# Optimization experiments

Measured on AMD Instinct MI355X. Metric: run time of the kernel, lower is better.

## Reference

```python
import jax, jax.numpy as jnp
import numpy as np
import math

MAXL = 2; C = 16; A = 32; B = 2; LAYERS = 2; CUT = 0.5


def _cg_coeff(l1, l2, l, m1, m2, m):
    if m1 + m2 != m or l < abs(l1 - l2) or l > l1 + l2:
        return 0.0
    f = math.factorial
    pre = math.sqrt((2 * l + 1) * f(l + l1 - l2) * f(l - l1 + l2) * f(l1 + l2 - l) / f(l1 + l2 + l + 1))
    pre *= math.sqrt(f(l + m) * f(l - m) * f(l1 + m1) * f(l1 - m1) * f(l2 + m2) * f(l2 - m2))
    s = 0.0
    for k in range(0, l1 + l2 + 1):
        d = (k, l1 + l2 - l - k, l1 - m1 - k, l2 + m2 - k, l - l2 + m1 + k, l - l1 - m2 + k)
        if min(d) < 0:
            continue
        s += (-1.0) ** k / (f(d[0]) * f(d[1]) * f(d[2]) * f(d[3]) * f(d[4]) * f(d[5]))
    return pre * s


def _cg_matrix(l1, l2, l):
    M = np.zeros((2 * l1 + 1, 2 * l2 + 1, 2 * l + 1), dtype=np.float32)
    for m1 in range(-l1, l1 + 1):
        for m2 in range(-l2, l2 + 1):
            m = m1 + m2
            if -l <= m <= l:
                M[m1 + l1, m2 + l2, m + l] = _cg_coeff(l1, l2, l, m1, m2, m)
    return M

_CG = {}
for _l1 in range(MAXL + 1):
    for _l2 in range(MAXL + 1):
        for _l in range(abs(_l1 - _l2), min(_l1 + _l2, MAXL) + 1):
            _CG[(_l1, _l2, _l)] = jnp.asarray(_cg_matrix(_l1, _l2, _l))


def _cg_product(parts1, parts2):
    # GElib-style CG product: channel dim is the outer product of input channels,
    # concatenated over valid (l1,l2) couplings in loop order.
    out = [[] for _ in range(MAXL + 1)]
    for l1, p1 in enumerate(parts1):
        for l2, p2 in enumerate(parts2):
            for l in range(abs(l1 - l2), min(l1 + l2, MAXL) + 1):
                t = jnp.einsum('xyz,...xc,...yd->...zcd', _CG[(l1, l2, l)], p1, p2)
                out[l].append(t.reshape(t.shape[:-2] + (t.shape[-2] * t.shape[-1],)))
    return [jnp.concatenate(o, axis=-1) for o in out]


def _sph(rel_pos):
    # Real spherical harmonics (orthonormal convention) of the normalized rel vector,
    # broadcast across the C channels of type_sph.
    eps = 1e-6
    r = jnp.sqrt(jnp.sum(rel_pos * rel_pos, axis=-1, keepdims=True) + eps)
    u = rel_pos / r
    x, y, z = u[..., 0], u[..., 1], u[..., 2]
    Y0 = 0.28209479 * jnp.ones_like(x)[..., None]
    Y1 = 0.48860251 * jnp.stack([y, z, x], axis=-1)
    Y2 = jnp.stack([1.09254843 * x * y, 1.09254843 * y * z,
                    0.31539157 * (3.0 * z * z - 1.0), 1.09254843 * x * z,
                    0.54627422 * (x * x - y * y)], axis=-1)
    return [jnp.repeat(Y[..., None], C, axis=-1) for Y in (Y0, Y1, Y2)]


def _cg_layer(parts, conn, sph, wnl, wrel):
    # message pass: masked neighbor sum (Rmask1 gather)
    mp = [jnp.einsum('bij,bjomc->biomc', conn, p) for p in parts]
    cg_nl = _cg_product(mp, mp)
    mixed_nl = [jnp.einsum('baomt,aotc->baomc', p, w) for p, w in zip(cg_nl, wnl)]
    rep = [jnp.tile(p, (1, 1, A, 1, 1)) for p in mixed_nl]  # adims [A,1] -> [A,A]
    cg_rel = _cg_product(rep, sph)
    mixed_rel = [jnp.einsum('bijmt,ijtc->bijmc', p, w) for p, w in zip(cg_rel, wrel)]
    return [jnp.sum(p, axis=2, keepdims=True) for p in mixed_rel]


def _scalars(parts):
    b, a = parts[0].shape[0], parts[0].shape[1]
    s0 = parts[0].reshape(b, a, C)
    sn = [jnp.einsum('baomc,baomd->bacd', p, p).reshape(b, a, C * C) for p in parts]
    return jnp.concatenate([s0] + sn, axis=-1)


def setup_inputs() -> dict:
    key = jax.random.key(0)
    ks = jax.random.split(key, 20)
    tau_nl = [3 * C * C, 6 * C * C, 6 * C * C]
    inp = {
        'v0': jax.random.normal(ks[0], (B, A, 1, 1, C), jnp.float32),
        'v1': jax.random.normal(ks[1], (B, A, 1, 3, C), jnp.float32),
        'v2': jax.random.normal(ks[2], (B, A, 1, 5, C), jnp.float32),
        'rel_pos': jax.random.normal(ks[3], (B, A, A, 3), jnp.float32),
        'norms': jax.random.uniform(ks[4], (B, A, A), jnp.float32),
    }
    i = 5
    for layer in range(LAYERS):
        for l in range(MAXL + 1):
            inp['wnl%d_%d' % (layer, l)] = 0.02 * jax.random.normal(ks[i], (A, 1, tau_nl[l], C), jnp.float32); i += 1
            inp['wrel%d_%d' % (layer, l)] = 0.02 * jax.random.normal(ks[i], (A, A, tau_nl[l], C), jnp.float32); i += 1
    return inp


def reference(v0, v1, v2, rel_pos, norms,
              wnl0_0, wrel0_0, wnl0_1, wrel0_1, wnl0_2, wrel0_2,
              wnl1_0, wrel1_0, wnl1_1, wrel1_1, wnl1_2, wrel1_2):
    parts = [v0, v1, v2]
    sph = _sph(rel_pos)
    conn = (norms < CUT).astype(v0.dtype)
    wnl = [[wnl0_0, wnl0_1, wnl0_2], [wnl1_0, wnl1_1, wnl1_2]]
    wrel = [[wrel0_0, wrel0_1, wrel0_2], [wrel1_0, wrel1_1, wrel1_2]]
    outs = []
    for L in range(LAYERS):
        parts = _cg_layer(parts, conn, sph, wnl[L], wrel[L])
        outs.append(_scalars(parts))
    return jnp.concatenate(outs, axis=0)
```

## Files before the change

kernel.cpp:

```cpp
#include <hip/hip_runtime.h>

#define NA 32
#define NB 2
#define NC 16

constexpr int KL1[15]   = {0,1,2, 0,1,1,1,2,2, 0,1,1,2,2,2};
constexpr int KL2[15]   = {0,1,2, 1,0,1,2,1,2, 2,1,2,0,1,2};
constexpr int KOFF[15]  = {0,1,10, 35,44,53,80,125,170, 245,270,315,390,415,490};
constexpr int KLBASE[3] = {0,3,9};
constexpr int KLOFF[3]  = {0,1,4};
constexpr int KOFF3[3]  = {0,1024,4096};
__constant__ int CP_L1[15]   = {0,1,2, 0,1,1,1,2,2, 0,1,1,2,2,2};
__constant__ int CP_L2[15]   = {0,1,2, 1,0,1,2,1,2, 2,1,2,0,1,2};
__constant__ int CP_OFF[15]  = {0,1,10, 35,44,53,80,125,170, 245,270,315,390,415,490};
__constant__ int LBASE[3] = {0,3,9};
__constant__ int LOFF[3]  = {0,1,4};
__constant__ int OFF3[3]  = {0,1024,4096};

constexpr double cfact(int n){ double r=1.0; for(int i=2;i<=n;++i) r*=(double)i; return r; }
constexpr double csqrt(double x){
    double g = (x > 1.0) ? x : 1.0, prev = 0.0;
    for (int i = 0; i < 60 && g != prev; ++i) { prev = g; g = 0.5*(g + x/g); }
    return g;
}
struct CGT { float v[616]; };
constexpr CGT build_cg() {
    CGT t{};
    for (int cp=0; cp<15; ++cp){
        int l1=KL1[cp], l2=KL2[cp];
        int l = (cp<3)?0:((cp<9)?1:2);
        int n1=2*l1+1, n2=2*l2+1, nl=2*l+1;
        for (int x=0;x<n1;++x) for(int y=0;y<n2;++y) for(int z=0;z<nl;++z){
            int m1=x-l1, m2=y-l2, m=z-l;
            double val=0.0;
            if (m1+m2==m){
                double pre = csqrt((2.0*l+1.0)*cfact(l+l1-l2)*cfact(l-l1+l2)*cfact(l1+l2-l)/cfact(l1+l2+l+1));
                pre *= csqrt(cfact(l+m)*cfact(l-m)*cfact(l1+m1)*cfact(l1-m1)*cfact(l2+m2)*cfact(l2-m2));
                double s=0.0;
                for(int k=0;k<=l1+l2;++k){
                    int d0=k,d1=l1+l2-l-k,d2=l1-m1-k,d3=l2+m2-k,d4=l-l2+m1+k,d5=l-l1-m2+k;
                    if(d0<0||d1<0||d2<0||d3<0||d4<0||d5<0) continue;
                    double term = 1.0/(cfact(d0)*cfact(d1)*cfact(d2)*cfact(d3)*cfact(d4)*cfact(d5));
                    s += (k & 1) ? -term : term;
                }
                val = pre*s;
            }
            t.v[KOFF[cp] + (x*n2+y)*nl + z] = (float)val;
        }
    }
    return t;
}
__constant__ CGT CGC = build_cg();

template<int L>
__device__ void nl_body(int i, int b, int z,
    const float* __restrict__ p0, const float* __restrict__ p1, const float* __restrict__ p2,
    const float* __restrict__ norms, const float* __restrict__ wnl,
    float* __restrict__ mnl, float* smem)
{
    constexpr int MD  = 2*L+1;
    constexpr int TAU = (L == 0) ? 768 : 1536;
    constexpr int NK  = TAU / 256;

    float* shCG = smem;
    float* mp   = smem + 616;
    float* shcg = mp + 144;
    float* red  = shcg + TAU;

    const int tid = threadIdx.x;
    const int wave = tid >> 6, lane = tid & 63;

    for (int e = tid; e < 616; e += 256) shCG[e] = CGC.v[e];

    if (tid < 144) {
        int xt = tid >> 4, c = tid & 15;
        int lp = (xt < 1) ? 0 : ((xt < 4) ? 1 : 2);
        int x = xt - KLOFF[lp];
        int md = 2*lp+1;
        const float* pp = (lp == 0) ? p0 : ((lp == 1) ? p1 : p2);
        const float* nr = norms + (b*NA + i)*NA;
        float s = 0.0f;
#pragma unroll
        for (int j = 0; j < NA; ++j) {
            float msk = (nr[j] < 0.5f) ? 1.0f : 0.0f;
            s += msk * pp[((b*NA + j)*md + x)*NC + c];
        }
        mp[tid] = s;
    }
    __syncthreads();

    {
        const int c = tid >> 4, d = tid & 15;
#pragma unroll
        for (int k = 0; k < NK; ++k) {
            const int cp = KLBASE[L] + k;
            const int l1 = KL1[cp], l2 = KL2[cp];
            const int n1 = 2*l1+1, n2 = 2*l2+1;
            float s = 0.0f;
#pragma unroll
            for (int x = 0; x < n1; ++x) {
                float mv = mp[(KLOFF[l1] + x)*NC + c];
#pragma unroll
                for (int y = 0; y < n2; ++y)
                    s += shCG[KOFF[cp] + (x*n2 + y)*MD + z] * mv * mp[(KLOFF[l2] + y)*NC + d];
            }
            shcg[k*256 + tid] = s;
        }
    }
    __syncthreads();

    {
        constexpr int PER = TAU / 4;
        constexpr int IT  = PER / 16;
        const int t_low = lane >> 2, c4 = lane & 3;
        const float4* w4 = (const float4*)(wnl + (size_t)i * TAU * 16);
        float4 acc = make_float4(0.f, 0.f, 0.f, 0.f);
        const int tb = wave * PER + t_low;
#pragma unroll 4
        for (int it = 0; it < IT; ++it) {
            int t = tb + it * 16;
            float sc = shcg[t];
            float4 wv = w4[t * 4 + c4];
            acc.x += sc * wv.x; acc.y += sc * wv.y; acc.z += sc * wv.z; acc.w += sc * wv.w;
        }
#pragma unroll
        for (int m = 4; m <= 32; m <<= 1) {
            acc.x += __shfl_xor(acc.x, m); acc.y += __shfl_xor(acc.y, m);
            acc.z += __shfl_xor(acc.z, m); acc.w += __shfl_xor(acc.w, m);
        }
        float4* red4 = (float4*)red;
        if (lane < 4) red4[wave * 4 + lane] = acc;
    }
    __syncthreads();
    if (tid < 16) {
        const float4* red4 = (const float4*)red;
        int c4 = tid >> 2, comp = tid & 3;
        float s = 0.0f;
#pragma unroll
        for (int w = 0; w < 4; ++w) s += ((const float*)&red4[w * 4 + c4])[comp];
        mnl[KOFF3[L] + ((b*NA + i)*MD + z)*NC + tid] = s;
    }
}

__device__ void scal_body(int b, int a, const float* __restrict__ pin,
                          float* __restrict__ out, float* sp)
{
    const int tid = threadIdx.x;
    for (int e = tid; e < 9*NC; e += 256) {
        int xt = e / NC, c = e % NC;
        int lp = (xt < 1) ? 0 : ((xt < 4) ? 1 : 2);
        sp[e] = pin[OFF3[lp] + ((b*NA + a)*(2*lp+1) + (xt - LOFF[lp]))*NC + c];
    }
    __syncthreads();
    float* orow = out + (size_t)(b*NA + a)*784;
    for (int e = tid; e < 784; e += 256) {
        float v;
        if (e < 16) {
            v = sp[e];
        } else {
            int g = e - 16;
            int lb = g >> 8; int c = (g >> 4) & 15; int d = g & 15;
            int md = 2*lb+1;
            float s = 0.0f;
            for (int zz = 0; zz < md; ++zz)
                s += sp[(LOFF[lb] + zz)*NC + c] * sp[(LOFF[lb] + zz)*NC + d];
            v = s;
        }
        orow[e] = v;
    }
}

__global__ __launch_bounds__(256) void k_nl(
    const float* __restrict__ p0, const float* __restrict__ p1, const float* __restrict__ p2,
    const float* __restrict__ norms,
    const float* __restrict__ w0, const float* __restrict__ w1, const float* __restrict__ w2,
    float* __restrict__ mnl, float* __restrict__ po,
    const float* __restrict__ prev_po, float* __restrict__ prev_out)
{
    __shared__ __align__(16) float smem[2360];
    const int bx = blockIdx.x;
    if (bx >= 576) {
        if (prev_po) {
            int sidx = bx - 576;
            scal_body(sidx >> 5, sidx & 31, prev_po, prev_out, smem);
        }
        return;
    }
    if (threadIdx.x < 16) po[bx*16 + threadIdx.x] = 0.0f;

    const int lq = bx >> 5, i = bx & 31;
    if (lq < 2)      nl_body<0>(i, lq, 0, p0, p1, p2, norms, w0, mnl, smem);
    else if (lq < 8) { int g = lq - 2; nl_body<1>(i, g/3, g%3, p0, p1, p2, norms, w1, mnl, smem); }
    else             { int g = lq - 8; nl_body<2>(i, g/5, g%5, p0, p1, p2, norms, w2, mnl, smem); }
}

template<int L>
__device__ void rel_body(int i, int jq, int half,
    const float* __restrict__ wr, const float* __restrict__ mnl,
    const float* __restrict__ relpos, float* __restrict__ pout,
    float* smem)
{
    constexpr int MD  = 2*L+1;
    constexpr int NBZ = 2*MD;
    constexpr int TAU = (L==0) ? 768 : 1536;
    constexpr int P   = (L==2) ? 5 : 8;

    float*  shCG = smem;
    float*  shY  = smem + 616;
    float*  shM  = shY + 72;
    float*  shG  = shM + 288;
    float4* shR  = (float4*)(shG + 4*48*NBZ);

    const int tid = threadIdx.x;
    const int wave = tid >> 6, lane = tid & 63;

    for (int e = tid; e < 616; e += 256) shCG[e] = CGC.v[e];

    if (tid < 8) {
        int jj = tid >> 1, b = tid & 1;
        int j = (jq << 2) + jj;
        const float* rp = relpos + (((size_t)(b*NA + i))*NA + j)*3;
        float px = rp[0], py = rp[1], pz = rp[2];
        float rr = sqrtf(px*px + py*py + pz*pz + 1e-6f);
        float ux = px/rr, uy = py/rr, uz = pz/rr;
        float* Y = shY + tid*9;
        Y[0] = 0.28209479f;
        Y[1] = 0.48860251f*uy; Y[2] = 0.48860251f*uz; Y[3] = 0.48860251f*ux;
        Y[4] = 1.09254843f*ux*uy; Y[5] = 1.09254843f*uy*uz;
        Y[6] = 0.31539157f*(3.0f*uz*uz - 1.0f);
        Y[7] = 1.09254843f*ux*uz; Y[8] = 0.54627422f*(ux*ux - uy*uy);
    }
    for (int e = tid; e < NB*9*NC; e += 256) {
        int b = e / (9*NC); int rem = e % (9*NC);
        int xt = rem / NC;  int c = rem % NC;
        int lp = (xt < 1) ? 0 : ((xt < 4) ? 1 : 2);
        shM[e] = mnl[OFF3[lp] + ((b*NA + i)*(2*lp+1) + (xt - LOFF[lp]))*NC + c];
    }
    __syncthreads();

    for (int e = tid; e < 4*48*NBZ; e += 256) {
        int q = e % NBZ; int r = (e/NBZ) % 48; int jj = e / (NBZ*48);
        int b = q / MD, z = q % MD;
        int R = half*48 + r; int k = R >> 4, c = R & 15;
        int cp = LBASE[L] + k;
        int l1 = CP_L1[cp], l2 = CP_L2[cp];
        int n1 = 2*l1+1, n2 = 2*l2+1;
        const float* cgp = shCG + CP_OFF[cp];
        float s = 0.0f;
        for (int x = 0; x < n1; ++x) {
            float mv = shM[(b*9 + LOFF[l1] + x)*NC + c];
            for (int y = 0; y < n2; ++y)
                s += cgp[(x*n2 + y)*MD + z] * mv * shY[((jj<<1)+b)*9 + LOFF[l2] + y];
        }
        shG[e] = s;
    }
    __syncthreads();

    const float* wbase = wr + ((size_t)(i*NA + (jq<<2))*TAU + half*(TAU/2))*16;
    const float* tb = wbase + tid*4;

    float4 buf[P];
#pragma unroll
    for (int c = 0; c < P; ++c)
        buf[c] = *(const float4*)(tb + (size_t)(c/12)*TAU*16 + (c%12)*1024);

    float4 acc[NBZ];
#pragma unroll
    for (int q = 0; q < NBZ; ++q) acc[q] = make_float4(0.f,0.f,0.f,0.f);

#pragma unroll
    for (int c = 0; c < 48; ++c) {
        const float4 v = buf[c % P];
        if (c + P < 48)
            buf[c % P] = *(const float4*)(tb + (size_t)((c+P)/12)*TAU*16 + ((c+P)%12)*1024);
        const int jj = c/12, r = (c%12)*4 + wave;
        const float* gp = shG + (jj*48 + r)*NBZ;
        float g[NBZ];
#pragma unroll
        for (int q = 0; q < NBZ; ++q) g[q] = gp[q];
#pragma unroll
        for (int q = 0; q < NBZ; ++q) {
            acc[q].x += g[q]*v.x; acc[q].y += g[q]*v.y;
            acc[q].z += g[q]*v.z; acc[q].w += g[q]*v.w;
        }
    }

#pragma unroll
    for (int q = 0; q < NBZ; ++q) {
        float4 v = acc[q];
#pragma unroll
        for (int m = 4; m <= 32; m <<= 1) {
            v.x += __shfl_xor(v.x, m); v.y += __shfl_xor(v.y, m);
            v.z += __shfl_xor(v.z, m); v.w += __shfl_xor(v.w, m);
        }
        acc[q] = v;
    }
    if (lane < 4) {
#pragma unroll
        for (int q = 0; q < NBZ; ++q) shR[(wave*4 + lane)*NBZ + q] = acc[q];
    }
    __syncthreads();
    for (int e = tid; e < NBZ*16; e += 256) {
        int q = e >> 4, cp = e & 15, qq = cp >> 2, cc = cp & 3;
        float s = 0.0f;
        for (int w = 0; w < 4; ++w) {
            const float* pr = (const float*)&shR[(w*4 + qq)*NBZ + q];
            s += pr[cc];
        }
        int b = q / MD, z = q % MD;
        atomicAdd(&pout[OFF3[L] + ((b*NA + i)*MD + z)*NC + cp], s);
    }
}

__global__ __launch_bounds__(256, 5) void k_rel(
    const float* __restrict__ mnl, const float* __restrict__ relpos,
    const float* __restrict__ wr0, const float* __restrict__ wr1, const float* __restrict__ wr2,
    float* __restrict__ pout)
{
    __shared__ __align__(16) float smem[3536];
    const int bx = blockIdx.x;
    const int s = bx >> 8, idx = bx & 255;
    const int i = idx >> 3, jq = idx & 7;
    if (s == 0)      rel_body<0>(i, jq, 0, wr0, mnl, relpos, pout, smem);
    else if (s == 1) rel_body<1>(i, jq, 0, wr1, mnl, relpos, pout, smem);
    else if (s == 2) rel_body<1>(i, jq, 1, wr1, mnl, relpos, pout, smem);
    else if (s == 3) rel_body<2>(i, jq, 0, wr2, mnl, relpos, pout, smem);
    else             rel_body<2>(i, jq, 1, wr2, mnl, relpos, pout, smem);
}

__global__ __launch_bounds__(256) void k_scal(const float* __restrict__ pin, float* __restrict__ out)
{
    __shared__ float sp[9*NC];
    scal_body(blockIdx.x >> 5, blockIdx.x & 31, pin, out, sp);
}

extern "C" void kernel_launch(void* const* d_in, const int* in_sizes, int n_in,
                              void* d_out, int out_size, void* d_ws, size_t ws_size,
                              hipStream_t stream)
{
    const float* v0     = (const float*)d_in[0];
    const float* v1     = (const float*)d_in[1];
    const float* v2     = (const float*)d_in[2];
    const float* relpos = (const float*)d_in[3];
    const float* norms  = (const float*)d_in[4];
    const float* wnl[2][3] = {
        {(const float*)d_in[5],  (const float*)d_in[7],  (const float*)d_in[9]},
        {(const float*)d_in[11], (const float*)d_in[13], (const float*)d_in[15]}};
    const float* wrel[2][3] = {
        {(const float*)d_in[6],  (const float*)d_in[8],  (const float*)d_in[10]},
        {(const float*)d_in[12], (const float*)d_in[14], (const float*)d_in[16]}};

    float* ws  = (float*)d_ws;
    float* mnl = ws;
    float* pA  = ws + 9216;
    float* pB  = ws + 18432;
    float* out = (float*)d_out;

    k_nl<<<640, 256, 0, stream>>>(v0, v1, v2, norms,
                                  wnl[0][0], wnl[0][1], wnl[0][2], mnl, pA,
                                  nullptr, nullptr);
    k_rel<<<1280, 256, 0, stream>>>(mnl, relpos, wrel[0][0], wrel[0][1], wrel[0][2], pA);
    k_nl<<<640, 256, 0, stream>>>(pA, pA + 1024, pA + 4096, norms,
                                  wnl[1][0], wnl[1][1], wnl[1][2], mnl, pB,
                                  pA, out);
    k_rel<<<1280, 256, 0, stream>>>(mnl, relpos, wrel[1][0], wrel[1][1], wrel[1][2], pB);
    k_scal<<<64, 256, 0, stream>>>(pB, out + (size_t)NB * NA * 784);
}
```

Before: 496.9 us.

## Pre-reduce relative weights over the redundant channel axis before the rel kernel

The spherical-harmonic factor is identical across its channel copies, so the weight tensor can be summed over that inner channel index first without changing the result. A new streaming kernel, k_wred, does this reduction into workspace once per layer. The rel kernel is rewritten as k_rel2, which runs on the smaller reduced weights with fewer blocks and no half-splitting. This cuts the redundant contraction work inside the rel stage. In exchange it adds two extra launches and a large workspace requirement, and it falls back to the old path when the workspace is too small.

```diff
diff --git a/kernel.cpp b/kernel.cpp
--- a/kernel.cpp
+++ b/kernel.cpp
@@ -194,22 +194,43 @@
     else             { int g = lq - 8; nl_body<2>(i, g/5, g%5, p0, p1, p2, norms, w2, mnl, smem); }
 }
 
+__global__ __launch_bounds__(256) void k_wred(
+    const float* __restrict__ s0, const float* __restrict__ s1, const float* __restrict__ s2,
+    float* __restrict__ dst)
+{
+    const int b = blockIdx.x, tid = threadIdx.x;
+    const float* src; size_t lrow, obase;
+    if (b < 768)       { src = s0; lrow = (size_t)b*64;        obase = 0u;        }
+    else if (b < 2304) { src = s1; lrow = (size_t)(b-768)*64;  obase = 786432u;   }
+    else               { src = s2; lrow = (size_t)(b-2304)*64; obase = 2359296u;  }
+    const size_t row = lrow + (size_t)(tid >> 2);
+    const int c4 = tid & 3;
+    const float4* sp = (const float4*)(src + row*256) + c4;
+    float4 a = sp[0];
+#pragma unroll
+    for (int d = 1; d < 16; ++d) {
+        float4 v = sp[(size_t)d*4];
+        a.x += v.x; a.y += v.y; a.z += v.z; a.w += v.w;
+    }
+    ((float4*)(dst + obase + row*16))[c4] = a;
+}
+
 template<int L>
-__device__ void rel_body(int i, int jq, int half,
+__device__ void rel_body2(int i, int jq,
     const float* __restrict__ wr, const float* __restrict__ mnl,
     const float* __restrict__ relpos, float* __restrict__ pout,
     float* smem)
 {
     constexpr int MD  = 2*L+1;
     constexpr int NBZ = 2*MD;
-    constexpr int TAU = (L==0) ? 768 : 1536;
-    constexpr int P   = (L==2) ? 5 : 8;
+    constexpr int NR  = (L==0) ? 48 : 96;
+    constexpr int RB  = NR/16;
 
     float*  shCG = smem;
-    float*  shY  = smem + 616;
+    float*  shY  = shCG + 616;
     float*  shM  = shY + 72;
     float*  shG  = shM + 288;
-    float4* shR  = (float4*)(shG + 4*48*NBZ);
+    float4* shR  = (float4*)(shG + 4*NR*NBZ);
 
     const int tid = threadIdx.x;
     const int wave = tid >> 6, lane = tid & 63;
@@ -238,6 +259,131 @@
     }
     __syncthreads();
 
+    for (int e = tid; e < 4*NR*NBZ; e += 256) {
+        int q = e % NBZ; int R = (e/NBZ) % NR; int jj = e / (NBZ*NR);
+        int b = q / MD, z = q % MD;
+        int k = R >> 4, c = R & 15;
+        int cp = LBASE[L] + k;
+        int l1 = CP_L1[cp], l2 = CP_L2[cp];
+        int n1 = 2*l1+1, n2 = 2*l2+1;
+        const float* cgp = shCG + CP_OFF[cp];
+        float s = 0.0f;
+        for (int x = 0; x < n1; ++x) {
+            float mv = shM[(b*9 + LOFF[l1] + x)*NC + c];
+            for (int y = 0; y < n2; ++y)
+                s += cgp[(x*n2 + y)*MD + z] * mv * shY[((jj<<1)+b)*9 + LOFF[l2] + y];
+        }
+        shG[e] = s;
+    }
+    __syncthreads();
+
+    const float* wbase = wr + (size_t)(i*NA + (jq<<2)) * NR * 16;
+    const int rloc = lane >> 2;
+    float4 acc[NBZ];
+#pragma unroll
+    for (int q = 0; q < NBZ; ++q) acc[q] = make_float4(0.f,0.f,0.f,0.f);
+
+#pragma unroll
+    for (int tt = 0; tt < RB; ++tt) {
+        const int T = tt*4 + wave;
+        const int jj = T / RB, rb = T % RB;
+        const float4 wv = ((const float4*)(wbase + ((size_t)(jj*NR) + rb*16)*16))[lane];
+        const float* gp = shG + ((size_t)(jj*NR) + rb*16 + rloc)*NBZ;
+        float g[NBZ];
+#pragma unroll
+        for (int q = 0; q < NBZ; ++q) g[q] = gp[q];
+#pragma unroll
+        for (int q = 0; q < NBZ; ++q) {
+            acc[q].x += g[q]*wv.x; acc[q].y += g[q]*wv.y;
+            acc[q].z += g[q]*wv.z; acc[q].w += g[q]*wv.w;
+        }
+    }
+
+#pragma unroll
+    for (int q = 0; q < NBZ; ++q) {
+        float4 v = acc[q];
+#pragma unroll
+        for (int m = 4; m <= 32; m <<= 1) {
+            v.x += __shfl_xor(v.x, m); v.y += __shfl_xor(v.y, m);
+            v.z += __shfl_xor(v.z, m); v.w += __shfl_xor(v.w, m);
+        }
+        acc[q] = v;
+    }
+    if (lane < 4) {
+#pragma unroll
+        for (int q = 0; q < NBZ; ++q) shR[(wave*4 + lane)*NBZ + q] = acc[q];
+    }
+    __syncthreads();
+    for (int e = tid; e < NBZ*16; e += 256) {
+        int q = e >> 4, cp = e & 15, qq = cp >> 2, cc = cp & 3;
+        float s = 0.0f;
+        for (int w = 0; w < 4; ++w) {
+            const float* pr = (const float*)&shR[(w*4 + qq)*NBZ + q];
+            s += pr[cc];
+        }
+        int b = q / MD, z = q % MD;
+        atomicAdd(&pout[OFF3[L] + ((b*NA + i)*MD + z)*NC + cp], s);
+    }
+}
+
+__global__ __launch_bounds__(256) void k_rel2(
+    const float* __restrict__ mnl, const float* __restrict__ relpos,
+    const float* __restrict__ w0, const float* __restrict__ w1, const float* __restrict__ w2,
+    float* __restrict__ pout)
+{
+    __shared__ __align__(16) float smem[5456];
+    const int bx = blockIdx.x;
+    const int s = bx >> 8, idx = bx & 255;
+    const int i = idx >> 3, jq = idx & 7;
+    if (s == 0)      rel_body2<0>(i, jq, w0, mnl, relpos, pout, smem);
+    else if (s == 1) rel_body2<1>(i, jq, w1, mnl, relpos, pout, smem);
+    else             rel_body2<2>(i, jq, w2, mnl, relpos, pout, smem);
+}
+
+template<int L>
+__device__ void rel_body_full(int i, int jq, int half,
+    const float* __restrict__ wr, const float* __restrict__ mnl,
+    const float* __restrict__ relpos, float* __restrict__ pout,
+    float* smem)
+{
+    constexpr int MD  = 2*L+1;
+    constexpr int NBZ = 2*MD;
+    constexpr int TAU = (L==0) ? 768 : 1536;
+    constexpr int P   = (L==2) ? 5 : 8;
+
+    float*  shCG = smem;
+    float*  shY  = smem + 616;
+    float*  shM  = shY + 72;
+    float*  shG  = shM + 288;
+    float4* shR  = (float4*)(shG + 4*48*NBZ);
+
+    const int tid = threadIdx.x;
+    const int wave = tid >> 6, lane = tid & 63;
+
+    for (int e = tid; e < 616; e += 256) shCG[e] = CGC.v[e];
+
+    if (tid < 8) {
+        int jj = tid >> 1, b = tid & 1;
+        int j = (jq << 2) + jj;
+        const float* rp = relpos + (((size_t)(b*NA + i))*NA + j)*3;
+        float px = rp[0], py = rp[1], pz = rp[2];
+        float rr = sqrtf(px*px + py*py + pz*pz + 1e-6f);
+        float ux = px/rr, uy = py/rr, uz = pz/rr;
+        float* Y = shY + tid*9;
+        Y[0] = 0.28209479f;
+        Y[1] = 0.48860251f*uy; Y[2] = 0.48860251f*uz; Y[3] = 0.48860251f*ux;
+        Y[4] = 1.09254843f*ux*uy; Y[5] = 1.09254843f*uy*uz;
+        Y[6] = 0.31539157f*(3.0f*uz*uz - 1.0f);
+        Y[7] = 1.09254843f*ux*uz; Y[8] = 0.54627422f*(ux*ux - uy*uy);
+    }
+    for (int e = tid; e < NB*9*NC; e += 256) {
+        int b = e / (9*NC); int rem = e % (9*NC);
+        int xt = rem / NC;  int c = rem % NC;
+        int lp = (xt < 1) ? 0 : ((xt < 4) ? 1 : 2);
+        shM[e] = mnl[OFF3[lp] + ((b*NA + i)*(2*lp+1) + (xt - LOFF[lp]))*NC + c];
+    }
+    __syncthreads();
+
     for (int e = tid; e < 4*48*NBZ; e += 256) {
         int q = e % NBZ; int r = (e/NBZ) % 48; int jj = e / (NBZ*48);
         int b = q / MD, z = q % MD;
@@ -312,7 +458,7 @@
     }
 }
 
-__global__ __launch_bounds__(256, 5) void k_rel(
+__global__ __launch_bounds__(256, 5) void k_rel_full(
     const float* __restrict__ mnl, const float* __restrict__ relpos,
     const float* __restrict__ wr0, const float* __restrict__ wr1, const float* __restrict__ wr2,
     float* __restrict__ pout)
@@ -321,11 +467,11 @@
     const int bx = blockIdx.x;
     const int s = bx >> 8, idx = bx & 255;
     const int i = idx >> 3, jq = idx & 7;
-    if (s == 0)      rel_body<0>(i, jq, 0, wr0, mnl, relpos, pout, smem);
-    else if (s == 1) rel_body<1>(i, jq, 0, wr1, mnl, relpos, pout, smem);
-    else if (s == 2) rel_body<1>(i, jq, 1, wr1, mnl, relpos, pout, smem);
-    else if (s == 3) rel_body<2>(i, jq, 0, wr2, mnl, relpos, pout, smem);
-    else             rel_body<2>(i, jq, 1, wr2, mnl, relpos, pout, smem);
+    if (s == 0)      rel_body_full<0>(i, jq, 0, wr0, mnl, relpos, pout, smem);
+    else if (s == 1) rel_body_full<1>(i, jq, 0, wr1, mnl, relpos, pout, smem);
+    else if (s == 2) rel_body_full<1>(i, jq, 1, wr1, mnl, relpos, pout, smem);
+    else if (s == 3) rel_body_full<2>(i, jq, 0, wr2, mnl, relpos, pout, smem);
+    else             rel_body_full<2>(i, jq, 1, wr2, mnl, relpos, pout, smem);
 }
 
 __global__ __launch_bounds__(256) void k_scal(const float* __restrict__ pin, float* __restrict__ out)
@@ -354,15 +500,35 @@
     float* mnl = ws;
     float* pA  = ws + 9216;
     float* pB  = ws + 18432;
+    float* wred = ws + 27648;
     float* out = (float*)d_out;
 
-    k_nl<<<640, 256, 0, stream>>>(v0, v1, v2, norms,
-                                  wnl[0][0], wnl[0][1], wnl[0][2], mnl, pA,
-                                  nullptr, nullptr);
-    k_rel<<<1280, 256, 0, stream>>>(mnl, relpos, wrel[0][0], wrel[0][1], wrel[0][2], pA);
-    k_nl<<<640, 256, 0, stream>>>(pA, pA + 1024, pA + 4096, norms,
-                                  wnl[1][0], wnl[1][1], wnl[1][2], mnl, pB,
-                                  pA, out);
-    k_rel<<<1280, 256, 0, stream>>>(mnl, relpos, wrel[1][0], wrel[1][1], wrel[1][2], pB);
-    k_scal<<<64, 256, 0, stream>>>(pB, out + (size_t)NB * NA * 784);
-}
+    const size_t WRED_FLOATS = 3932160;
+    const bool fast = ws_size >= (size_t)(27648 + WRED_FLOATS) * sizeof(float);
+
+    if (fast) {
+        k_wred<<<3840, 256, 0, stream>>>(wrel[0][0], wrel[0][1], wrel[0][2], wred);
+        k_nl<<<640, 256, 0, stream>>>(v0, v1, v2, norms,
+                                      wnl[0][0], wnl[0][1], wnl[0][2], mnl, pA,
+                                      nullptr, nullptr);
+        k_rel2<<<768, 256, 0, stream>>>(mnl, relpos,
+                                        wred, wred + 786432, wred + 2359296, pA);
+        k_wred<<<3840, 256, 0, stream>>>(wrel[1][0], wrel[1][1], wrel[1][2], wred);
+        k_nl<<<640, 256, 0, stream>>>(pA, pA + 1024, pA + 4096, norms,
+                                      wnl[1][0], wnl[1][1], wnl[1][2], mnl, pB,
+                                      pA, out);
+        k_rel2<<<768, 256, 0, stream>>>(mnl, relpos,
+                                        wred, wred + 786432, wred + 2359296, pB);
+        k_scal<<<64, 256, 0, stream>>>(pB, out + (size_t)NB * NA * 784);
+    } else {
+        k_nl<<<640, 256, 0, stream>>>(v0, v1, v2, norms,
+                                      wnl[0][0], wnl[0][1], wnl[0][2], mnl, pA,
+                                      nullptr, nullptr);
+        k_rel_full<<<1280, 256, 0, stream>>>(mnl, relpos, wrel[0][0], wrel[0][1], wrel[0][2], pA);
+        k_nl<<<640, 256, 0, stream>>>(pA, pA + 1024, pA + 4096, norms,
+                                      wnl[1][0], wnl[1][1], wnl[1][2], mnl, pB,
+                                      pA, out);
+        k_rel_full<<<1280, 256, 0, stream>>>(mnl, relpos, wrel[1][0], wrel[1][1], wrel[1][2], pB);
+        k_scal<<<64, 256, 0, stream>>>(pB, out + (size_t)NB * NA * 784);
+    }
+}
```

After: 516.1 us. 1.04x slower.
